# Performance work log

Measured on AMD Instinct MI355X. Metric: run time of the kernel, lower is better.

Reference implementation:

```python
import jax, jax.numpy as jnp
from jax import lax
import numpy as np

B, C, N, T, K = 16, 64, 512, 64, 2
KSIZE, DIL = 2, 1
PAD = (KSIZE - 1) * DIL
EPS = 1e-5


def _powers(A, k):
    Ps = [jnp.eye(A.shape[0], dtype=A.dtype)]
    for _ in range(k):
        Ps.append(Ps[-1] @ A)
    return jnp.stack(Ps)  # (K+1, N, N)


def setup_inputs() -> dict:
    key = jax.random.key(0)
    ks = jax.random.split(key, 12)
    x = jax.random.normal(ks[0], (B, C, N, T), dtype=jnp.float32)
    # row-normalized random transition matrices, precomputed powers
    Af = jax.random.uniform(ks[1], (N, N), dtype=jnp.float32)
    Af = Af / Af.sum(axis=1, keepdims=True)
    Ab = Af.T / Af.T.sum(axis=1, keepdims=True)
    Aa = jax.random.uniform(ks[2], (N, N), dtype=jnp.float32)
    Aa = Aa / Aa.sum(axis=1, keepdims=True)
    P_f_pows = _powers(Af, K)
    P_b_pows = _powers(Ab, K)
    A_adp_pows = _powers(Aa, K)
    s = 0.05
    filter_w = jax.random.normal(ks[3], (C, C, 1, KSIZE), dtype=jnp.float32) * s
    filter_b = jnp.zeros((C,), jnp.float32)
    gate_w = jax.random.normal(ks[4], (C, C, 1, KSIZE), dtype=jnp.float32) * s
    gate_b = jnp.zeros((C,), jnp.float32)
    skip_w = jax.random.normal(ks[5], (C, C, 1, 1), dtype=jnp.float32) * s
    skip_b = jnp.zeros((C,), jnp.float32)
    weight_f = jax.random.normal(ks[6], (K + 1, C, C), dtype=jnp.float32) * s
    weight_b = jax.random.normal(ks[7], (K + 1, C, C), dtype=jnp.float32) * s
    gcn_bias = jnp.zeros((C,), jnp.float32)
    ln_gamma = jnp.ones((C,), jnp.float32)
    ln_beta = jnp.zeros((C,), jnp.float32)
    alpha = jnp.float32(0.5)
    return dict(x=x, P_f_pows=P_f_pows, P_b_pows=P_b_pows, A_adp_pows=A_adp_pows,
                filter_w=filter_w, filter_b=filter_b, gate_w=gate_w, gate_b=gate_b,
                skip_w=skip_w, skip_b=skip_b, weight_f=weight_f, weight_b=weight_b,
                gcn_bias=gcn_bias, ln_gamma=ln_gamma, ln_beta=ln_beta, alpha=alpha)


def _conv(x, w, b, dil=1):
    y = lax.conv_general_dilated(x, w, window_strides=(1, 1), padding='VALID',
                                 rhs_dilation=(1, dil),
                                 dimension_numbers=('NCHW', 'OIHW', 'NCHW'))
    return y + b[None, :, None, None]


def _apply_powers(xt, P_pows, weights):
    # xt: (B*T, N, Cin); P_pows: (K+1, N, N); weights: (K+1, Cin, Cout)
    xk = jnp.einsum('kij,bjc->kbic', P_pows, xt)
    return jnp.einsum('kbic,kco->bio', xk, weights)


def reference(x, P_f_pows, P_b_pows, A_adp_pows,
              filter_w, filter_b, gate_w, gate_b, skip_w, skip_b,
              weight_f, weight_b, gcn_bias, ln_gamma, ln_beta, alpha):
    # --- Gated TCN (causal left-pad along time) ---
    x_pad = jnp.pad(x, ((0, 0), (0, 0), (0, 0), (PAD, 0)))
    f = jnp.tanh(_conv(x_pad, filter_w, filter_b, DIL))
    g = jax.nn.sigmoid(_conv(x_pad, gate_w, gate_b, DIL))
    out = f * g                                   # (B, C, N, T)
    skip = _conv(out, skip_w, skip_b)             # 1x1 conv
    x_temporal = x + out                          # in_channels == out_channels

    # --- Diffusion GCN on (B*T, N, C) ---
    xt = jnp.transpose(x_temporal, (0, 3, 2, 1)).reshape(B * T, N, C)
    static_out = (_apply_powers(xt, P_f_pows, weight_f)
                  + _apply_powers(xt, P_b_pows, weight_b)
                  + gcn_bias[None, None, :])
    adapt_out = (_apply_powers(xt, A_adp_pows, weight_f)
                 + _apply_powers(xt, A_adp_pows, weight_b)
                 + gcn_bias[None, None, :])

    a = jax.nn.sigmoid(alpha)
    x_gcn = a * static_out + (1.0 - a) * adapt_out

    # --- LayerNorm over channel dim (dropout = identity in eval) ---
    mu = x_gcn.mean(axis=-1, keepdims=True)
    var = ((x_gcn - mu) ** 2).mean(axis=-1, keepdims=True)
    x_gcn = (x_gcn - mu) * lax.rsqrt(var + EPS) * ln_gamma + ln_beta

    x_out = x_gcn.reshape(B, T, N, C).transpose(0, 3, 2, 1)  # (B, C, N, T)
    return (x_out, skip)
```

## Files before the change

### kernel.cpp

```cpp
#include <hip/hip_runtime.h>
#include <cstdint>
#include <cstddef>

#define NB 16
#define NC 64
#define NN 512
#define NT 64
#define BT (NB*NT)
#define NN2 (NN*NN)
#define XSTRIDE_B (NC*NN*NT)
#define XSTRIDE_C (NN*NT)
#define XT_ROW (BT*NC)

typedef __attribute__((ext_vector_type(8))) short short8;
typedef __attribute__((ext_vector_type(4))) float f32x4;
typedef unsigned short ushort_t;
typedef unsigned int uint_t;

__device__ __forceinline__ ushort_t f2bf(float f) {
    uint_t u = __builtin_bit_cast(uint_t, f);
    u += 0x7FFFu + ((u >> 16) & 1u);
    return (ushort_t)(u >> 16);
}
__device__ __forceinline__ float bf2f(ushort_t u) {
    return __builtin_bit_cast(float, (uint_t)u << 16);
}
__device__ __forceinline__ void gl_lds16(const void* g, void* s) {
    __builtin_amdgcn_global_load_lds(
        (const __attribute__((address_space(1))) unsigned int*)g,
        (__attribute__((address_space(3))) unsigned int*)s, 16, 0, 0);
}
__device__ __forceinline__ void wait_vm(int n) {
    if (n >= 7)      asm volatile("s_waitcnt vmcnt(7)" ::: "memory");
    else if (n == 5) asm volatile("s_waitcnt vmcnt(5)" ::: "memory");
    else if (n == 4) asm volatile("s_waitcnt vmcnt(4)" ::: "memory");
    else if (n == 3) asm volatile("s_waitcnt vmcnt(3)" ::: "memory");
    else if (n == 2) asm volatile("s_waitcnt vmcnt(2)" ::: "memory");
    else             asm volatile("s_waitcnt vmcnt(0)" ::: "memory");
}

__global__ void k_prep(const float* __restrict__ wf, const float* __restrict__ wb,
                       const float* __restrict__ alpha, ushort_t* __restrict__ Wcb) {
    int i = blockIdx.x * 256 + threadIdx.x;
    if (i >= 7 * 4096) return;
    float a = 1.f / (1.f + expf(-alpha[0]));
    int r = i >> 12, co = i & 4095;
    int c = co >> 6, o = co & 63;
    float v;
    if      (r == 0) v = wf[co] + wb[co];
    else if (r == 1) v = a * wf[4096 + co];
    else if (r == 2) v = a * wf[8192 + co];
    else if (r == 3) v = a * wb[4096 + co];
    else if (r == 4) v = a * wb[8192 + co];
    else if (r == 5) v = (1.f - a) * (wf[4096 + co] + wb[4096 + co]);
    else             v = (1.f - a) * (wf[8192 + co] + wb[8192 + co]);
    int chunk = ((c >> 5) << 2) | (o >> 4);
    int lane  = (((c >> 3) & 3) << 4) | (o & 15);
    int j     = c & 7;
    Wcb[r * 4096 + chunk * 512 + lane * 8 + j] = f2bf(v);
}

__global__ void k_prepP(const float* __restrict__ Pf, const float* __restrict__ Pb,
                        const float* __restrict__ Aa, ushort_t* __restrict__ Apk) {
    int i = blockIdx.x * 256 + threadIdx.x;
    if (i >= 196608) return;
    int lane = i & 63, kc = (i >> 6) & 15, nt = (i >> 10) & 31, r = i >> 15;
    const float* base;
    if      (r == 0) base = Pf + NN2;
    else if (r == 1) base = Pf + 2 * NN2;
    else if (r == 2) base = Pb + NN2;
    else if (r == 3) base = Pb + 2 * NN2;
    else if (r == 4) base = Aa + NN2;
    else             base = Aa + 2 * NN2;
    int n = nt * 16 + (lane & 15);
    int k0 = kc * 32 + (lane >> 4) * 8;
    const float* src = base + (size_t)n * NN + k0;
    float4 v0 = ((const float4*)src)[0];
    float4 v1 = ((const float4*)src)[1];
    uint4 o;
    o.x = (uint_t)f2bf(v0.x) | ((uint_t)f2bf(v0.y) << 16);
    o.y = (uint_t)f2bf(v0.z) | ((uint_t)f2bf(v0.w) << 16);
    o.z = (uint_t)f2bf(v1.x) | ((uint_t)f2bf(v1.y) << 16);
    o.w = (uint_t)f2bf(v1.z) | ((uint_t)f2bf(v1.w) << 16);
    *(uint4*)(Apk + (size_t)i * 8) = o;
}

__global__ void k_prepW(const float* __restrict__ fw, const float* __restrict__ gw,
                        const float* __restrict__ sw, ushort_t* __restrict__ Wt) {
    int i = blockIdx.x * 256 + threadIdx.x;
    if (i >= 5 * 4096) return;
    int mat = i >> 12, t = i & 4095;
    int chunk = t >> 9, l = (t >> 3) & 63, j = t & 7;
    int m = chunk >> 1, kb = chunk & 1;
    int o = m * 16 + (l & 15);
    int c = kb * 32 + ((l >> 4) << 3) + j;
    float v;
    if      (mat == 0) v = fw[o * 128 + c * 2 + 0];
    else if (mat == 1) v = fw[o * 128 + c * 2 + 1];
    else if (mat == 2) v = gw[o * 128 + c * 2 + 0];
    else if (mat == 3) v = gw[o * 128 + c * 2 + 1];
    else               v = sw[o * 64 + c];
    Wt[i] = f2bf(v);
}

#define XS_P 72
__device__ __forceinline__ int swzA(int r, int c) {
    return r * XS_P + (c ^ (((r >> 4) & 3) << 3));
}
__global__ __launch_bounds__(256, 3) void k_tcn(
    const float* __restrict__ x,
    const ushort_t* __restrict__ Wt,
    const float* __restrict__ fb, const float* __restrict__ gb,
    const float* __restrict__ sb,
    float* __restrict__ skip_out, ushort_t* __restrict__ XTbf) {
    __shared__ __align__(16) ushort_t Xs[65 * XS_P];
    __shared__ __align__(16) ushort_t Os[64 * XS_P];

    int tx = threadIdx.x;
    int b = blockIdx.x >> 9, n = blockIdx.x & (NN - 1);

    {
        int c = tx >> 2, tq = tx & 3, t0 = tq * 16;
        const float* src = x + (size_t)b * XSTRIDE_B + (size_t)c * XSTRIDE_C
                             + (size_t)n * NT + t0;
        float4 v0 = ((const float4*)src)[0];
        float4 v1 = ((const float4*)src)[1];
        float4 v2 = ((const float4*)src)[2];
        float4 v3 = ((const float4*)src)[3];
        float vv[16] = {v0.x, v0.y, v0.z, v0.w, v1.x, v1.y, v1.z, v1.w,
                        v2.x, v2.y, v2.z, v2.w, v3.x, v3.y, v3.z, v3.w};
#pragma unroll
        for (int e = 0; e < 16; ++e) {
            int r = t0 + e + 1;
            Xs[swzA(r, c)] = f2bf(vv[e]);
        }
        if (tx < 8) ((uint4*)Xs)[tx] = (uint4){0, 0, 0, 0};
    }
    __syncthreads();

    int w = tx >> 6, l = tx & 63, lr = l & 15, lg = l >> 4;

    short8 wf0[2], wf1[2], wg0[2], wg1[2], wsk[2];
#pragma unroll
    for (int kb = 0; kb < 2; ++kb) {
        int off = (w * 2 + kb) * 512 + l * 8;
        wf0[kb] = *(const short8*)(Wt + 0 * 4096 + off);
        wf1[kb] = *(const short8*)(Wt + 1 * 4096 + off);
        wg0[kb] = *(const short8*)(Wt + 2 * 4096 + off);
        wg1[kb] = *(const short8*)(Wt + 3 * 4096 + off);
        wsk[kb] = *(const short8*)(Wt + 4 * 4096 + off);
    }
    float fbv[4], gbv[4], sbv[4];
#pragma unroll
    for (int q = 0; q < 4; ++q) {
        int o = w * 16 + lg * 4 + q;
        fbv[q] = fb[o]; gbv[q] = gb[o]; sbv[q] = sb[o];
    }

#pragma unroll
    for (int tb = 0; tb < 4; ++tb) {
        short8 b0[2], b1[2];
#pragma unroll
        for (int kb = 0; kb < 2; ++kb) {
            int blk = kb * 4 + lg;
            int r1 = tb * 16 + lr + 1, r0 = tb * 16 + lr;
            b1[kb] = *(const short8*)&Xs[r1 * XS_P + (((blk ^ ((r1 >> 4) & 3)) << 3))];
            b0[kb] = *(const short8*)&Xs[r0 * XS_P + (((blk ^ ((r0 >> 4) & 3)) << 3))];
        }
        f32x4 aF = {fbv[0], fbv[1], fbv[2], fbv[3]};
        f32x4 aG = {gbv[0], gbv[1], gbv[2], gbv[3]};
        aF = __builtin_amdgcn_mfma_f32_16x16x32_bf16(wf0[0], b0[0], aF, 0, 0, 0);
        aF = __builtin_amdgcn_mfma_f32_16x16x32_bf16(wf0[1], b0[1], aF, 0, 0, 0);
        aF = __builtin_amdgcn_mfma_f32_16x16x32_bf16(wf1[0], b1[0], aF, 0, 0, 0);
        aF = __builtin_amdgcn_mfma_f32_16x16x32_bf16(wf1[1], b1[1], aF, 0, 0, 0);
        aG = __builtin_amdgcn_mfma_f32_16x16x32_bf16(wg0[0], b0[0], aG, 0, 0, 0);
        aG = __builtin_amdgcn_mfma_f32_16x16x32_bf16(wg0[1], b0[1], aG, 0, 0, 0);
        aG = __builtin_amdgcn_mfma_f32_16x16x32_bf16(wg1[0], b1[0], aG, 0, 0, 0);
        aG = __builtin_amdgcn_mfma_f32_16x16x32_bf16(wg1[1], b1[1], aG, 0, 0, 0);
        int t = tb * 16 + lr;
#pragma unroll
        for (int q = 0; q < 4; ++q) {
            float fo = tanhf(aF[q]);
            float go = 1.f / (1.f + expf(-aG[q]));
            int o = w * 16 + lg * 4 + q;
            Os[swzA(t, o)] = f2bf(fo * go);
        }
    }
    __syncthreads();

    float* skp = skip_out + (size_t)b * XSTRIDE_B + (size_t)n * NT;
#pragma unroll
    for (int tb = 0; tb < 4; ++tb) {
        int t = tb * 16 + lr;
        short8 ov[2];
#pragma unroll
        for (int kb = 0; kb < 2; ++kb) {
            int blk = kb * 4 + lg;
            ov[kb] = *(const short8*)&Os[t * XS_P + (((blk ^ ((t >> 4) & 3)) << 3))];
        }
        f32x4 aS = {sbv[0], sbv[1], sbv[2], sbv[3]};
        aS = __builtin_amdgcn_mfma_f32_16x16x32_bf16(wsk[0], ov[0], aS, 0, 0, 0);
        aS = __builtin_amdgcn_mfma_f32_16x16x32_bf16(wsk[1], ov[1], aS, 0, 0, 0);
#pragma unroll
        for (int q = 0; q < 4; ++q) {
            int o = w * 16 + lg * 4 + q;
            skp[(size_t)o * XSTRIDE_C + t] = aS[q];
        }
    }

    {
        int t = tx >> 2, cch = (tx & 3) * 16;
        ushort_t* dst = XTbf + (size_t)n * XT_ROW + (size_t)b * 4096 + t * 64 + cch;
        int rX = t + 1;
#pragma unroll
        for (int blk2 = 0; blk2 < 2; ++blk2) {
            int cb = (cch >> 3) + blk2;
            short8 xv = *(const short8*)&Xs[rX * XS_P + ((cb ^ ((rX >> 4) & 3)) << 3)];
            short8 ovv = *(const short8*)&Os[t * XS_P + ((cb ^ ((t >> 4) & 3)) << 3)];
            uint_t pk[4];
#pragma unroll
            for (int h = 0; h < 4; ++h) {
                float s0 = bf2f((ushort_t)xv[h * 2]) + bf2f((ushort_t)ovv[h * 2]);
                float s1 = bf2f((ushort_t)xv[h * 2 + 1]) + bf2f((ushort_t)ovv[h * 2 + 1]);
                pk[h] = (uint_t)f2bf(s0) | ((uint_t)f2bf(s1) << 16);
            }
            *(uint4*)(dst + blk2 * 8) = (uint4){pk[0], pk[1], pk[2], pk[3]};
        }
    }
}

__global__ __launch_bounds__(256) void k_tr(const ushort_t* __restrict__ XTbf,
                                            ushort_t* __restrict__ Bpk) {
    __shared__ ushort_t tile[32 * XS_P];
    int tx = threadIdx.x;
    int bt = blockIdx.x;
    int jj = tx >> 3, c8 = (tx & 7) * 8;
    int f = tx >> 6, lane = tx & 63, lg = lane >> 4, lr = lane & 15;
    for (int kc = 0; kc < 16; ++kc) {
        if (kc) __syncthreads();
        *(uint4*)&tile[jj * XS_P + c8] =
            *(const uint4*)(XTbf + (size_t)(kc * 32 + jj) * XT_ROW + bt * 64 + c8);
        __syncthreads();
        ushort_t vals[8];
#pragma unroll
        for (int e = 0; e < 8; ++e)
            vals[e] = tile[(lg * 8 + e) * XS_P + f * 16 + lr];
        uint4 o;
        o.x = (uint_t)vals[0] | ((uint_t)vals[1] << 16);
        o.y = (uint_t)vals[2] | ((uint_t)vals[3] << 16);
        o.z = (uint_t)vals[4] | ((uint_t)vals[5] << 16);
        o.w = (uint_t)vals[6] | ((uint_t)vals[7] << 16);
        *(uint4*)(Bpk + (size_t)bt * 32768 + kc * 2048 + tx * 8) = o;
    }
}

__global__ __launch_bounds__(256, 3) void k_gcn(
    const ushort_t* __restrict__ Apk,
    const ushort_t* __restrict__ Bpk,
    const ushort_t* __restrict__ XTbf,
    const ushort_t* __restrict__ Wcb,
    const float* __restrict__ bias,
    ushort_t* __restrict__ G) {
    __shared__ __align__(16) ushort_t sB[4][2048];
    __shared__ __align__(16) ushort_t sY[4][16 * 72];
    __shared__ __align__(16) float sC[2][4][64][4];

    int tx = threadIdx.x;
    int w = tx >> 6, l = tx & 63;
    int lr = l & 15, lg = l >> 4;
    int s = w >> 1, h = w & 1;

    int bid = (blockIdx.x & 7) * 2048 + (blockIdx.x >> 3);
    int bt = bid >> 4;
    int n0i = bid & 15;
    int n0 = n0i << 5;

    f32x4 acc[3][4];
#pragma unroll
    for (int j = 0; j < 3; ++j)
#pragma unroll
        for (int f = 0; f < 4; ++f) acc[j][f] = (f32x4){0.f, 0.f, 0.f, 0.f};

    const ushort_t* aBase = Apk + (size_t)(h * 3) * NN2
                                + (size_t)(n0i * 2 + s) * 8192 + l * 8;
    const ushort_t* bSrc = Bpk + (size_t)bt * 32768 + w * 512 + l * 8;

    short8 aE[3], aO[3];
#pragma unroll
    for (int j = 0; j < 3; ++j) aE[j] = *(const short8*)(aBase + (size_t)j * NN2);
#pragma unroll
    for (int d = 0; d < 3; ++d)
        gl_lds16(bSrc + d * 2048, &sB[d][w * 512]);
    wait_vm(2);
    __builtin_amdgcn_s_barrier();
    __builtin_amdgcn_sched_barrier(0);

#pragma unroll
    for (int tt = 0; tt < 8; ++tt) {
        {
            const int t = 2 * tt;
            if (t + 1 < 16) {
#pragma unroll
                for (int j = 0; j < 3; ++j)
                    aO[j] = *(const short8*)(aBase + (size_t)j * NN2 + (t + 1) * 512);
            }
            if (t + 3 < 16)
                gl_lds16(bSrc + (t + 3) * 2048, &sB[(t + 3) & 3][w * 512]);
            const ushort_t* sBr = &sB[t & 3][0];
            __builtin_amdgcn_s_setprio(1);
            short8 bv[4];
#pragma unroll
            for (int f = 0; f < 4; ++f)
                bv[f] = *(const short8*)(sBr + f * 512 + l * 8);
#pragma unroll
            for (int j = 0; j < 3; ++j)
#pragma unroll
                for (int f = 0; f < 4; ++f)
                    acc[j][f] = __builtin_amdgcn_mfma_f32_16x16x32_bf16(
                        aE[j], bv[f], acc[j][f], 0, 0, 0);
            __builtin_amdgcn_s_setprio(0);
            wait_vm(t <= 12 ? 5 : (t == 13 ? 4 : (t == 14 ? 3 : 0)));
            __builtin_amdgcn_s_barrier();
            __builtin_amdgcn_sched_barrier(0);
        }
        {
            const int t = 2 * tt + 1;
            if (t + 1 < 16) {
#pragma unroll
                for (int j = 0; j < 3; ++j)
                    aE[j] = *(const short8*)(aBase + (size_t)j * NN2 + (t + 1) * 512);
            }
            if (t + 3 < 16)
                gl_lds16(bSrc + (t + 3) * 2048, &sB[(t + 3) & 3][w * 512]);
            const ushort_t* sBr = &sB[t & 3][0];
            __builtin_amdgcn_s_setprio(1);
            short8 bv[4];
#pragma unroll
            for (int f = 0; f < 4; ++f)
                bv[f] = *(const short8*)(sBr + f * 512 + l * 8);
#pragma unroll
            for (int j = 0; j < 3; ++j)
#pragma unroll
                for (int f = 0; f < 4; ++f)
                    acc[j][f] = __builtin_amdgcn_mfma_f32_16x16x32_bf16(
                        aO[j], bv[f], acc[j][f], 0, 0, 0);
            __builtin_amdgcn_s_setprio(0);
            wait_vm(t <= 12 ? 5 : (t == 13 ? 4 : (t == 14 ? 3 : 0)));
            __builtin_amdgcn_s_barrier();
            __builtin_amdgcn_sched_barrier(0);
        }
    }

    f32x4 acc2[4];
#pragma unroll
    for (int fo = 0; fo < 4; ++fo) {
        float b = (h == 0) ? bias[fo * 16 + lr] : 0.f;
        acc2[fo] = (f32x4){b, b, b, b};
    }
    ushort_t* sYw = &sY[w][0];
    const ushort_t* wBase = Wcb + l * 8;

    if (h == 0) {
        const ushort_t* xs = XTbf + (size_t)(n0 + s * 16 + lr) * XT_ROW + bt * 64 + lg * 8;
        short8 ay0 = *(const short8*)(xs);
        short8 ay1 = *(const short8*)(xs + 32);
#pragma unroll
        for (int kh = 0; kh < 2; ++kh)
#pragma unroll
            for (int fo = 0; fo < 4; ++fo) {
                short8 wv = *(const short8*)(wBase + (kh * 4 + fo) * 512);
                acc2[fo] = __builtin_amdgcn_mfma_f32_16x16x32_bf16(
                    kh ? ay1 : ay0, wv, acc2[fo], 0, 0, 0);
            }
    }
#pragma unroll
    for (int j = 0; j < 3; ++j) {
        int wcIdx = (h == 0) ? (j + 1) : (j + 4);
#pragma unroll
        for (int f = 0; f < 4; ++f)
#pragma unroll
            for (int q = 0; q < 4; ++q)
                sYw[(lg * 4 + q) * 72 + f * 16 + lr] = f2bf(acc[j][f][q]);
        short8 ay0 = *(const short8*)(&sYw[lr * 72 + lg * 8]);
        short8 ay1 = *(const short8*)(&sYw[lr * 72 + 32 + lg * 8]);
#pragma unroll
        for (int kh = 0; kh < 2; ++kh)
#pragma unroll
            for (int fo = 0; fo < 4; ++fo) {
                short8 wv = *(const short8*)(wBase + wcIdx * 4096 + (kh * 4 + fo) * 512);
                acc2[fo] = __builtin_amdgcn_mfma_f32_16x16x32_bf16(
                    kh ? ay1 : ay0, wv, acc2[fo], 0, 0, 0);
            }
    }

    if (h == 1) {
#pragma unroll
        for (int fo = 0; fo < 4; ++fo)
            *(f32x4*)&sC[s][fo][l][0] = acc2[fo];
    }
    __syncthreads();
    if (h == 0) {
        ushort_t* gp = G + (size_t)(n0 + s * 16 + lg * 4) * XT_ROW + bt * 64 + lr;
#pragma unroll
        for (int fo = 0; fo < 4; ++fo) {
            f32x4 other = *(const f32x4*)&sC[s][fo][l][0];
#pragma unroll
            for (int q = 0; q < 4; ++q)
                gp[(size_t)q * XT_ROW + fo * 16] = f2bf(acc2[fo][q] + other[q]);
        }
    }
}

__global__ __launch_bounds__(256) void k_ln_t(
    const ushort_t* __restrict__ G,
    const float* __restrict__ gamma, const float* __restrict__ beta,
    float* __restrict__ xout) {
    __shared__ float sT[64 * 65];
    __shared__ float sMu[64], sRs[64];
    __shared__ float sS[64 * 4], sQ[64 * 4];

    int bid = blockIdx.x;
    int b = bid >> 9, n = bid & (NN - 1);
    int tx = threadIdx.x;
    const ushort_t* src = G + (size_t)n * XT_ROW + (size_t)b * (NT * NC);

#pragma unroll
    for (int u = 0; u < 2; ++u) {
        int fi = u * 256 + tx;
        uint4 v = ((const uint4*)src)[fi];
        int t = fi >> 3, c = (fi & 7) * 8;
        sT[t * 65 + c + 0] = bf2f((ushort_t)(v.x & 0xffff));
        sT[t * 65 + c + 1] = bf2f((ushort_t)(v.x >> 16));
        sT[t * 65 + c + 2] = bf2f((ushort_t)(v.y & 0xffff));
        sT[t * 65 + c + 3] = bf2f((ushort_t)(v.y >> 16));
        sT[t * 65 + c + 4] = bf2f((ushort_t)(v.z & 0xffff));
        sT[t * 65 + c + 5] = bf2f((ushort_t)(v.z >> 16));
        sT[t * 65 + c + 6] = bf2f((ushort_t)(v.w & 0xffff));
        sT[t * 65 + c + 7] = bf2f((ushort_t)(v.w >> 16));
    }
    __syncthreads();
    {
        int row = tx >> 2, seg = tx & 3;
        float s = 0.f, q = 0.f;
        for (int cc = 0; cc < 16; ++cc) {
            float v = sT[row * 65 + seg * 16 + cc];
            s += v; q += v * v;
        }
        sS[row * 4 + seg] = s; sQ[row * 4 + seg] = q;
    }
    __syncthreads();
    if (tx < 64) {
        float ss = sS[tx * 4] + sS[tx * 4 + 1] + sS[tx * 4 + 2] + sS[tx * 4 + 3];
        float qq = sQ[tx * 4] + sQ[tx * 4 + 1] + sQ[tx * 4 + 2] + sQ[tx * 4 + 3];
        float mu = ss * (1.f / 64.f);
        float var = qq * (1.f / 64.f) - mu * mu;
        sMu[tx] = mu; sRs[tx] = rsqrtf(var + 1e-5f);
    }
    __syncthreads();
    {
        int t = tx & 63, cg = (tx >> 6) * 16;
        float mu = sMu[t], rs = sRs[t];
        for (int cc = 0; cc < 16; ++cc) {
            int c = cg + cc;
            float v = (sT[t * 65 + c] - mu) * rs * gamma[c] + beta[c];
            xout[(size_t)b * XSTRIDE_B + (size_t)c * XSTRIDE_C + (size_t)n * NT + t] = v;
        }
    }
}

extern "C" void kernel_launch(void* const* d_in, const int* in_sizes, int n_in,
                              void* d_out, int out_size, void* d_ws, size_t ws_size,
                              hipStream_t stream) {
    const float* x     = (const float*)d_in[0];
    const float* Pf    = (const float*)d_in[1];
    const float* Pb    = (const float*)d_in[2];
    const float* Aa    = (const float*)d_in[3];
    const float* fw    = (const float*)d_in[4];
    const float* fb    = (const float*)d_in[5];
    const float* gw    = (const float*)d_in[6];
    const float* gb    = (const float*)d_in[7];
    const float* sw    = (const float*)d_in[8];
    const float* sb    = (const float*)d_in[9];
    const float* wf    = (const float*)d_in[10];
    const float* wb    = (const float*)d_in[11];
    const float* gbias = (const float*)d_in[12];
    const float* lng   = (const float*)d_in[13];
    const float* lnb   = (const float*)d_in[14];
    const float* alpha = (const float*)d_in[15];

    float* xout = (float*)d_out;
    float* skip = (float*)d_out + (size_t)NB * NC * NN * NT;

    char* ws = (char*)d_ws;
    ushort_t* XTbf = (ushort_t*)(ws);
    ushort_t* Bpk  = (ushort_t*)(ws + 67108864);
    ushort_t* Gb   = (ushort_t*)(ws + 134217728);
    ushort_t* Apk  = (ushort_t*)(ws + 201326592);
    ushort_t* Wcb  = (ushort_t*)(ws + 204472320);
    ushort_t* Wt   = (ushort_t*)(ws + 204537856);

    hipLaunchKernelGGL(k_prep, dim3(112), dim3(256), 0, stream, wf, wb, alpha, Wcb);
    hipLaunchKernelGGL(k_prepW, dim3(80), dim3(256), 0, stream, fw, gw, sw, Wt);
    hipLaunchKernelGGL(k_prepP, dim3(768), dim3(256), 0, stream, Pf, Pb, Aa, Apk);
    hipLaunchKernelGGL(k_tcn, dim3(NB * NN), dim3(256), 0, stream,
                       x, Wt, fb, gb, sb, skip, XTbf);
    hipLaunchKernelGGL(k_tr, dim3(1024), dim3(256), 0, stream, XTbf, Bpk);
    hipLaunchKernelGGL(k_gcn, dim3(16384), dim3(256), 0, stream,
                       Apk, Bpk, XTbf, Wcb, gbias, Gb);
    hipLaunchKernelGGL(k_ln_t, dim3(NB * NN), dim3(256), 0, stream, Gb, lng, lnb, xout);
}
```

Measured before the change: 403.1 us.

## Stage third A-power operand via LDS and alias shared buffers to raise occupancy

The GCN kernel now keeps only two A-operand fragments in registers and streams the third A power through a double-buffered LDS region with async global-to-LDS loads. The B, Y and C shared arrays are merged into one aliased 24KB buffer. Launch bounds go from 3 to 4 blocks per SM. The aim is to cut register pressure and LDS footprint so more waves can hide memory latency, at the cost of an extra LDS read per step and retuned vmcnt waits that may be fragile.

```diff
diff --git a/kernel.cpp b/kernel.cpp
--- a/kernel.cpp
+++ b/kernel.cpp
@@ -254,16 +254,14 @@
     }
 }
 
-__global__ __launch_bounds__(256, 3) void k_gcn(
+__global__ __launch_bounds__(256, 4) void k_gcn(
     const ushort_t* __restrict__ Apk,
     const ushort_t* __restrict__ Bpk,
     const ushort_t* __restrict__ XTbf,
     const ushort_t* __restrict__ Wcb,
     const float* __restrict__ bias,
     ushort_t* __restrict__ G) {
-    __shared__ __align__(16) ushort_t sB[4][2048];
-    __shared__ __align__(16) ushort_t sY[4][16 * 72];
-    __shared__ __align__(16) float sC[2][4][64][4];
+    __shared__ __align__(16) char smem[24576];
 
     int tx = threadIdx.x;
     int w = tx >> 6, l = tx & 63;
@@ -283,73 +281,68 @@
 
     const ushort_t* aBase = Apk + (size_t)(h * 3) * NN2
                                 + (size_t)(n0i * 2 + s) * 8192 + l * 8;
+    const ushort_t* a2Src = aBase + 2 * (size_t)NN2;
     const ushort_t* bSrc = Bpk + (size_t)bt * 32768 + w * 512 + l * 8;
 
-    short8 aE[3], aO[3];
-#pragma unroll
-    for (int j = 0; j < 3; ++j) aE[j] = *(const short8*)(aBase + (size_t)j * NN2);
+    short8 aE[2], aO[2];
+    aE[0] = *(const short8*)(aBase);
+    aE[1] = *(const short8*)(aBase + NN2);
+#pragma unroll
+    for (int d = 0; d < 2; ++d)
+        gl_lds16(a2Src + d * 512, smem + 16384 + d * 4096 + w * 1024);
 #pragma unroll
     for (int d = 0; d < 3; ++d)
-        gl_lds16(bSrc + d * 2048, &sB[d][w * 512]);
+        gl_lds16(bSrc + d * 2048, smem + d * 4096 + w * 1024);
     wait_vm(2);
     __builtin_amdgcn_s_barrier();
     __builtin_amdgcn_sched_barrier(0);
 
 #pragma unroll
-    for (int tt = 0; tt < 8; ++tt) {
-        {
-            const int t = 2 * tt;
-            if (t + 1 < 16) {
-#pragma unroll
-                for (int j = 0; j < 3; ++j)
-                    aO[j] = *(const short8*)(aBase + (size_t)j * NN2 + (t + 1) * 512);
+    for (int t = 0; t < 16; ++t) {
+        if (t + 1 < 16) {
+            if ((t & 1) == 0) {
+                aO[0] = *(const short8*)(aBase + (t + 1) * 512);
+                aO[1] = *(const short8*)(aBase + NN2 + (t + 1) * 512);
+            } else {
+                aE[0] = *(const short8*)(aBase + (t + 1) * 512);
+                aE[1] = *(const short8*)(aBase + NN2 + (t + 1) * 512);
             }
-            if (t + 3 < 16)
-                gl_lds16(bSrc + (t + 3) * 2048, &sB[(t + 3) & 3][w * 512]);
-            const ushort_t* sBr = &sB[t & 3][0];
-            __builtin_amdgcn_s_setprio(1);
-            short8 bv[4];
-#pragma unroll
-            for (int f = 0; f < 4; ++f)
-                bv[f] = *(const short8*)(sBr + f * 512 + l * 8);
-#pragma unroll
-            for (int j = 0; j < 3; ++j)
-#pragma unroll
-                for (int f = 0; f < 4; ++f)
-                    acc[j][f] = __builtin_amdgcn_mfma_f32_16x16x32_bf16(
-                        aE[j], bv[f], acc[j][f], 0, 0, 0);
-            __builtin_amdgcn_s_setprio(0);
-            wait_vm(t <= 12 ? 5 : (t == 13 ? 4 : (t == 14 ? 3 : 0)));
-            __builtin_amdgcn_s_barrier();
-            __builtin_amdgcn_sched_barrier(0);
-        }
-        {
-            const int t = 2 * tt + 1;
-            if (t + 1 < 16) {
-#pragma unroll
-                for (int j = 0; j < 3; ++j)
-                    aE[j] = *(const short8*)(aBase + (size_t)j * NN2 + (t + 1) * 512);
-            }
-            if (t + 3 < 16)
-                gl_lds16(bSrc + (t + 3) * 2048, &sB[(t + 3) & 3][w * 512]);
-            const ushort_t* sBr = &sB[t & 3][0];
-            __builtin_amdgcn_s_setprio(1);
-            short8 bv[4];
-#pragma unroll
-            for (int f = 0; f < 4; ++f)
-                bv[f] = *(const short8*)(sBr + f * 512 + l * 8);
-#pragma unroll
-            for (int j = 0; j < 3; ++j)
-#pragma unroll
-                for (int f = 0; f < 4; ++f)
-                    acc[j][f] = __builtin_amdgcn_mfma_f32_16x16x32_bf16(
-                        aO[j], bv[f], acc[j][f], 0, 0, 0);
-            __builtin_amdgcn_s_setprio(0);
-            wait_vm(t <= 12 ? 5 : (t == 13 ? 4 : (t == 14 ? 3 : 0)));
-            __builtin_amdgcn_s_barrier();
-            __builtin_amdgcn_sched_barrier(0);
-        }
-    }
+        }
+        if (t + 2 < 16)
+            gl_lds16(a2Src + (t + 2) * 512,
+                     smem + 16384 + ((t + 2) & 1) * 4096 + w * 1024);
+        if (t + 3 < 16)
+            gl_lds16(bSrc + (t + 3) * 2048,
+                     smem + ((t + 3) & 3) * 4096 + w * 1024);
+
+        const char* sBr = smem + (t & 3) * 4096;
+        short8 a2 = *(const short8*)(smem + 16384 + (t & 1) * 4096 + w * 1024 + l * 16);
+        short8 bv[4];
+#pragma unroll
+        for (int f = 0; f < 4; ++f)
+            bv[f] = *(const short8*)(sBr + f * 1024 + l * 16);
+
+        __builtin_amdgcn_s_setprio(1);
+        const short8 a0 = (t & 1) ? aO[0] : aE[0];
+        const short8 a1 = (t & 1) ? aO[1] : aE[1];
+#pragma unroll
+        for (int f = 0; f < 4; ++f)
+            acc[0][f] = __builtin_amdgcn_mfma_f32_16x16x32_bf16(a0, bv[f], acc[0][f], 0, 0, 0);
+#pragma unroll
+        for (int f = 0; f < 4; ++f)
+            acc[1][f] = __builtin_amdgcn_mfma_f32_16x16x32_bf16(a1, bv[f], acc[1][f], 0, 0, 0);
+#pragma unroll
+        for (int f = 0; f < 4; ++f)
+            acc[2][f] = __builtin_amdgcn_mfma_f32_16x16x32_bf16(a2, bv[f], acc[2][f], 0, 0, 0);
+        __builtin_amdgcn_s_setprio(0);
+
+        wait_vm(t <= 12 ? 5 : (t == 13 ? 4 : (t == 14 ? 2 : 0)));
+        __builtin_amdgcn_s_barrier();
+        __builtin_amdgcn_sched_barrier(0);
+    }
+
+    float* sC = (float*)smem;
+    ushort_t* sYw = (ushort_t*)(smem + 8192) + w * 1152;
 
     f32x4 acc2[4];
 #pragma unroll
@@ -357,7 +350,6 @@
         float b = (h == 0) ? bias[fo * 16 + lr] : 0.f;
         acc2[fo] = (f32x4){b, b, b, b};
     }
-    ushort_t* sYw = &sY[w][0];
     const ushort_t* wBase = Wcb + l * 8;
 
     if (h == 0) {
@@ -396,14 +388,14 @@
     if (h == 1) {
 #pragma unroll
         for (int fo = 0; fo < 4; ++fo)
-            *(f32x4*)&sC[s][fo][l][0] = acc2[fo];
+            *(f32x4*)&sC[(s * 4 + fo) * 256 + l * 4] = acc2[fo];
     }
     __syncthreads();
     if (h == 0) {
         ushort_t* gp = G + (size_t)(n0 + s * 16 + lg * 4) * XT_ROW + bt * 64 + lr;
 #pragma unroll
         for (int fo = 0; fo < 4; ++fo) {
-            f32x4 other = *(const f32x4*)&sC[s][fo][l][0];
+            f32x4 other = *(const f32x4*)&sC[(s * 4 + fo) * 256 + l * 4];
 #pragma unroll
             for (int q = 0; q < 4; ++q)
                 gp[(size_t)q * XT_ROW + fo * 16] = f2bf(acc2[fo][q] + other[q]);
```

Measured after the change: 402.4 us. About the same (-0.2%).
